# Kernel tuning notes

Hardware: AMD Instinct MI355X
Metric: run time of the kernel (lower is better)

## Reference

```python
import jax, jax.numpy as jnp
import numpy as np

B, V, FIN, K, FOUT, E = 8, 100000, 32, 4, 64, 800000


def setup_inputs() -> dict:
    key = jax.random.key(0)
    ks = jax.random.split(key, 6)
    inputs = jax.random.normal(ks[0], (B, V, FIN), dtype=jnp.float32)
    lap_rows = jax.random.randint(ks[1], (E,), 0, V, dtype=jnp.int32)
    lap_cols = jax.random.randint(ks[2], (E,), 0, V, dtype=jnp.int32)
    # rescaled-Laplacian nonzeros; small magnitude keeps the Chebyshev recurrence stable
    lap_vals = jax.random.normal(ks[3], (E,), dtype=jnp.float32) * 0.1
    # Kaiming-normal init: std = sqrt(2 / (Fin * K)) as in reset_parameters()
    std = float(np.sqrt(2.0 / (FIN * K)))
    weight = jax.random.normal(ks[4], (FIN, K, FOUT), dtype=jnp.float32) * std
    bias = jax.random.normal(ks[5], (FOUT,), dtype=jnp.float32) * 0.01
    return dict(inputs=inputs, lap_rows=lap_rows, lap_cols=lap_cols,
                lap_vals=lap_vals, weight=weight, bias=bias)


def reference(inputs, lap_rows, lap_cols, lap_vals, weight, bias):
    # inputs: [B, V, Fin]; weight: [Fin, K, Fout]; Laplacian in COO form.
    Bn, Vn, Fin = inputs.shape
    _, Kn, Fout = weight.shape

    def spmm(x):  # x: [V, Fin, B] -> L @ x via gather + segment-sum over edges
        msgs = lap_vals[:, None, None] * x[lap_cols]  # [E, Fin, B]
        return jax.ops.segment_sum(msgs, lap_rows, num_segments=Vn)

    x0 = jnp.transpose(inputs, (1, 2, 0))  # [V, Fin, B]
    xs = [x0]
    if Kn > 1:
        x1 = spmm(x0)
        xs.append(x1)
    for _ in range(2, Kn):
        x2 = 2.0 * spmm(x1) - x0  # Chebyshev recurrence T_k = 2 L T_{k-1} - T_{k-2}
        xs.append(x2)
        x0, x1 = x1, x2
    x = jnp.stack(xs, axis=0)  # [K, V, Fin, B]
    out = jnp.einsum('kvfb,fko->bvo', x, weight) + bias  # [B, V, Fout]
    return out
```

## Files before the change

kernel.cpp:

```cpp
#include <hip/hip_runtime.h>
#include <hip/hip_bf16.h>

#define B_    8
#define V_    100000
#define FIN_  32
#define K_    4
#define FOUT_ 64
#define E_    800000
#define NODE_F 256

typedef __attribute__((ext_vector_type(8))) short bf16x8;
typedef __attribute__((ext_vector_type(4))) float floatx4;

static __device__ inline float bf2f(unsigned short u) {
    unsigned int x = ((unsigned int)u) << 16;
    return __builtin_bit_cast(float, x);
}
static __device__ inline unsigned short f2bf(float f) {
    __hip_bfloat16 h = __float2bfloat16(f);
    return __builtin_bit_cast(unsigned short, h);
}

__global__ __launch_bounds__(256) void k_transpose(const float* __restrict__ in,
                                                   unsigned short* __restrict__ x0,
                                                   const int* __restrict__ rows,
                                                   int* __restrict__ counts,
                                                   const float* __restrict__ weight,
                                                   unsigned short* __restrict__ wpack) {
    int tid = blockIdx.x * 256 + threadIdx.x;
    int f4 = tid & 7;
    int m  = tid >> 3;
    int v  = m >> 3;
    int b  = m & 7;
    float4 val = ((const float4*)(in + ((size_t)b * V_ + v) * FIN_))[f4];
    ushort4 o;
    o.x = f2bf(val.x); o.y = f2bf(val.y); o.z = f2bf(val.z); o.w = f2bf(val.w);
    ((ushort4*)x0)[tid] = o;

    if (tid < E_) atomicAdd(&counts[rows[tid]], 1);

    if (tid < 1024) {
        int lane = tid & 63;
        int ot   = (tid >> 6) & 3;
        int kq   = tid >> 8;
        int quad = lane >> 4, l16 = lane & 15;
        bf16x8 w;
        #pragma unroll
        for (int j = 0; j < 8; ++j)
            w[j] = (short)f2bf(weight[(size_t)(quad * 8 + j) * (K_ * FOUT_) + kq * FOUT_ + ot * 16 + l16]);
        *((bf16x8*)(wpack + (size_t)tid * 8)) = w;
    }
}

__global__ __launch_bounds__(256) void k_zero_int(int* __restrict__ p, int n) {
    int t = blockIdx.x * 256 + threadIdx.x;
    if (t < n) p[t] = 0;
}

__global__ __launch_bounds__(1024) void k_scan1(const int* __restrict__ counts,
                                                int* __restrict__ row_ptr,
                                                int* __restrict__ cursor,
                                                int* __restrict__ bsums, int n) {
    __shared__ int s[1024];
    int t = threadIdx.x;
    int idx = blockIdx.x * 1024 + t;
    int v = (idx < n) ? counts[idx] : 0;
    s[t] = v;
    __syncthreads();
    for (int off = 1; off < 1024; off <<= 1) {
        int add = (t >= off) ? s[t - off] : 0;
        __syncthreads();
        s[t] += add;
        __syncthreads();
    }
    if (idx < n) {
        int r = s[t] - v;
        row_ptr[idx] = r;
        cursor[idx]  = r;
    }
    if (t == 1023) bsums[blockIdx.x] = s[1023];
}

__global__ __launch_bounds__(128) void k_scan2(const int* __restrict__ bsums,
                                               int* __restrict__ boffs, int nb) {
    __shared__ int s[128];
    int t = threadIdx.x;
    int v = (t < nb) ? bsums[t] : 0;
    s[t] = v;
    __syncthreads();
    for (int off = 1; off < 128; off <<= 1) {
        int add = (t >= off) ? s[t - off] : 0;
        __syncthreads();
        s[t] += add;
        __syncthreads();
    }
    boffs[t] = s[t] - v;
}

__global__ __launch_bounds__(256) void k_scatter(const int* __restrict__ rows,
                                                 const int* __restrict__ cols,
                                                 const float* __restrict__ vals,
                                                 int* __restrict__ cursor,
                                                 const int* __restrict__ boffs,
                                                 int2* __restrict__ e_pack) {
    int e = blockIdx.x * 256 + threadIdx.x;
    if (e < E_) {
        int r = rows[e];
        int pos = atomicAdd(&cursor[r], 1) + boffs[r >> 10];
        e_pack[pos] = make_int2(cols[e], __float_as_int(vals[e]));
    }
}

static __device__ inline void spmm_row(const unsigned short* __restrict__ xc,
                                       const int2* __restrict__ ep,
                                       int beg, int end, int lane, float a[4]) {
    int e = beg;
    for (; e + 3 < end; e += 4) {
        int2 p0 = ep[e], p1 = ep[e + 1], p2 = ep[e + 2], p3 = ep[e + 3];
        ushort4 g0 = *((const ushort4*)(xc + (size_t)p0.x * NODE_F + lane * 4));
        ushort4 g1 = *((const ushort4*)(xc + (size_t)p1.x * NODE_F + lane * 4));
        ushort4 g2 = *((const ushort4*)(xc + (size_t)p2.x * NODE_F + lane * 4));
        ushort4 g3 = *((const ushort4*)(xc + (size_t)p3.x * NODE_F + lane * 4));
        float w0 = __int_as_float(p0.y), w1 = __int_as_float(p1.y);
        float w2 = __int_as_float(p2.y), w3 = __int_as_float(p3.y);
        a[0] += w0 * bf2f(g0.x); a[1] += w0 * bf2f(g0.y); a[2] += w0 * bf2f(g0.z); a[3] += w0 * bf2f(g0.w);
        a[0] += w1 * bf2f(g1.x); a[1] += w1 * bf2f(g1.y); a[2] += w1 * bf2f(g1.z); a[3] += w1 * bf2f(g1.w);
        a[0] += w2 * bf2f(g2.x); a[1] += w2 * bf2f(g2.y); a[2] += w2 * bf2f(g2.z); a[3] += w2 * bf2f(g2.w);
        a[0] += w3 * bf2f(g3.x); a[1] += w3 * bf2f(g3.y); a[2] += w3 * bf2f(g3.z); a[3] += w3 * bf2f(g3.w);
    }
    for (; e < end; ++e) {
        int2 p = ep[e];
        ushort4 g = *((const ushort4*)(xc + (size_t)p.x * NODE_F + lane * 4));
        float w = __int_as_float(p.y);
        a[0] += w * bf2f(g.x); a[1] += w * bf2f(g.y); a[2] += w * bf2f(g.z); a[3] += w * bf2f(g.w);
    }
}

__global__ __launch_bounds__(256) void k_spmm(const unsigned short* __restrict__ xc,
                                              const unsigned short* __restrict__ xp,
                                              const int* __restrict__ row_ptr,
                                              const int* __restrict__ boffs,
                                              const int2* __restrict__ ep,
                                              unsigned short* __restrict__ xn,
                                              float scale, int has_prev) {
    int wave = threadIdx.x >> 6;
    int lane = threadIdx.x & 63;
    int v = blockIdx.x * 4 + wave;
    if (v >= V_) return;
    int beg = row_ptr[v] + boffs[v >> 10];
    int end = (v == V_ - 1) ? E_ : row_ptr[v + 1] + boffs[(v + 1) >> 10];

    float a[4] = {0.f, 0.f, 0.f, 0.f};
    spmm_row(xc, ep, beg, end, lane, a);

    float r[4];
    if (has_prev) {
        ushort4 p = *((const ushort4*)(xp + (size_t)v * NODE_F + lane * 4));
        r[0] = scale * a[0] - bf2f(p.x);
        r[1] = scale * a[1] - bf2f(p.y);
        r[2] = scale * a[2] - bf2f(p.z);
        r[3] = scale * a[3] - bf2f(p.w);
    } else {
        r[0] = a[0]; r[1] = a[1]; r[2] = a[2]; r[3] = a[3];
    }
    ushort4 o;
    o.x = f2bf(r[0]); o.y = f2bf(r[1]); o.z = f2bf(r[2]); o.w = f2bf(r[3]);
    *((ushort4*)(xn + (size_t)v * NODE_F + lane * 4)) = o;
}

__global__ __launch_bounds__(256) void k_spmm3c(const unsigned short* __restrict__ x0,
                                                const unsigned short* __restrict__ x1,
                                                const unsigned short* __restrict__ x2,
                                                const int* __restrict__ row_ptr,
                                                const int* __restrict__ boffs,
                                                const int2* __restrict__ ep,
                                                const unsigned short* __restrict__ wpack,
                                                const float* __restrict__ bias,
                                                float* __restrict__ out) {
    __shared__ __align__(16) unsigned short x3s[4][2][NODE_F];
    int wave = threadIdx.x >> 6;
    int lane = threadIdx.x & 63;
    int quad = lane >> 4;
    int l16  = lane & 15;
    int pair = blockIdx.x * 4 + wave;
    int v0 = pair * 2;

    #pragma unroll 1
    for (int s = 0; s < 2; ++s) {
        int v = v0 + s;
        int beg = row_ptr[v] + boffs[v >> 10];
        int end = (v == V_ - 1) ? E_ : row_ptr[v + 1] + boffs[(v + 1) >> 10];
        float a[4] = {0.f, 0.f, 0.f, 0.f};
        spmm_row(x2, ep, beg, end, lane, a);
        ushort4 p1 = *((const ushort4*)(x1 + (size_t)v * NODE_F + lane * 4));
        ushort4 o;
        o.x = f2bf(2.f * a[0] - bf2f(p1.x));
        o.y = f2bf(2.f * a[1] - bf2f(p1.y));
        o.z = f2bf(2.f * a[2] - bf2f(p1.z));
        o.w = f2bf(2.f * a[3] - bf2f(p1.w));
        *((ushort4*)&x3s[wave][s][lane * 4]) = o;
    }
    __syncthreads();

    const unsigned short* xs012[3] = {x0, x1, x2};
    bf16x8 wfrag[4][4];
    #pragma unroll
    for (int kq = 0; kq < 4; ++kq)
        #pragma unroll
        for (int ot = 0; ot < 4; ++ot)
            wfrag[kq][ot] = *((const bf16x8*)(wpack + (size_t)((kq * 4 + ot) * 64 + lane) * 8));

    floatx4 acc[4];
    #pragma unroll
    for (int ot = 0; ot < 4; ++ot)
        acc[ot] = *((const floatx4*)(bias + ot * 16 + quad * 4));

    int m0 = pair * 16;
    #pragma unroll
    for (int kq = 0; kq < 4; ++kq) {
        bf16x8 xf;
        if (kq < 3)
            xf = *((const bf16x8*)(xs012[kq] + (size_t)(m0 + l16) * FIN_ + quad * 8));
        else
            xf = *((const bf16x8*)&x3s[wave][l16 >> 3][(l16 & 7) * FIN_ + quad * 8]);
        #pragma unroll
        for (int ot = 0; ot < 4; ++ot)
            acc[ot] = __builtin_amdgcn_mfma_f32_16x16x32_bf16(wfrag[kq][ot], xf, acc[ot], 0, 0, 0);
    }

    int m = m0 + l16;
    int v = m >> 3;
    int b = m & 7;
    float* op = out + ((size_t)b * V_ + v) * FOUT_ + quad * 4;
    #pragma unroll
    for (int ot = 0; ot < 4; ++ot)
        *((floatx4*)(op + ot * 16)) = acc[ot];
}

extern "C" void kernel_launch(void* const* d_in, const int* in_sizes, int n_in,
                              void* d_out, int out_size, void* d_ws, size_t ws_size,
                              hipStream_t stream) {
    const float* inputs  = (const float*)d_in[0];
    const int*   laprows = (const int*)d_in[1];
    const int*   lapcols = (const int*)d_in[2];
    const float* lapvals = (const float*)d_in[3];
    const float* weight  = (const float*)d_in[4];
    const float* bias    = (const float*)d_in[5];
    float* out = (float*)d_out;

    const size_t XN = (size_t)V_ * NODE_F;
    unsigned short* x0 = (unsigned short*)d_ws;
    unsigned short* x1 = x0 + XN;
    unsigned short* x2 = x1 + XN;
    int* counts  = (int*)(x2 + XN);
    int* row_ptr = counts + V_;
    int* cursor  = row_ptr + V_;
    int* bsums   = cursor + V_;
    int* boffs   = bsums + 128;
    int2* e_pack = (int2*)(boffs + 128);
    unsigned short* wpack = (unsigned short*)(e_pack + E_);

    const int NB_SCAN = (V_ + 1023) / 1024;

    hipLaunchKernelGGL(k_zero_int, dim3((V_ + 255) / 256), dim3(256), 0, stream, counts, V_);
    hipLaunchKernelGGL(k_transpose, dim3((V_ * B_ * 8) / 256), dim3(256), 0, stream,
                       inputs, x0, laprows, counts, weight, wpack);
    hipLaunchKernelGGL(k_scan1, dim3(NB_SCAN), dim3(1024), 0, stream,
                       counts, row_ptr, cursor, bsums, V_);
    hipLaunchKernelGGL(k_scan2, dim3(1), dim3(128), 0, stream, bsums, boffs, NB_SCAN);
    hipLaunchKernelGGL(k_scatter, dim3((E_ + 255) / 256), dim3(256), 0, stream,
                       laprows, lapcols, lapvals, cursor, boffs, e_pack);

    hipLaunchKernelGGL(k_spmm, dim3(V_ / 4), dim3(256), 0, stream,
                       x0, (const unsigned short*)nullptr, row_ptr, boffs, e_pack, x1, 1.0f, 0);
    hipLaunchKernelGGL(k_spmm, dim3(V_ / 4), dim3(256), 0, stream,
                       x1, x0, row_ptr, boffs, e_pack, x2, 2.0f, 1);

    hipLaunchKernelGGL(k_spmm3c, dim3(12500), dim3(256), 0, stream,
                       x0, x1, x2, row_ptr, boffs, e_pack, wpack, bias, out);
}
```

Baseline: 608.8 us.

## Gather int8-quantized node features with per-node scales in SpMM

Each Chebyshev term is additionally stored as int8 with a per-node scale (offset by 128), and the SpMM gathers read these int8 rows instead of bf16, halving gathered bytes per edge. The zero-point is removed through a running sum of scaled edge weights. Bf16 copies are still written for the dense MFMA stage and the previous-term subtraction. Output stores become nontemporal. This adds a wave-wide max reduction and extra writes per node, and lowers gather precision to 8 bits, which risks accuracy tolerance.

Result: faster. 582.7 us (-4.3%).

```diff
diff --git a/kernel.cpp b/kernel.cpp
--- a/kernel.cpp
+++ b/kernel.cpp
@@ -21,13 +21,39 @@
     return __builtin_bit_cast(unsigned short, h);
 }
 
+static __device__ inline float wave_max64(float m) {
+    #pragma unroll
+    for (int off = 1; off < 64; off <<= 1)
+        m = fmaxf(m, __shfl_xor(m, off));
+    return m;
+}
+
+static __device__ inline void quant_store(const float r[4], int v, int lane,
+                                          unsigned char* __restrict__ xi,
+                                          float* __restrict__ sc) {
+    float m = fmaxf(fmaxf(fabsf(r[0]), fabsf(r[1])), fmaxf(fabsf(r[2]), fabsf(r[3])));
+    m = wave_max64(m);
+    float inv = (m > 0.f) ? 127.f / m : 0.f;
+    if (lane == 0) sc[v] = (m > 0.f) ? m * (1.f / 127.f) : 0.f;
+    unsigned int q = 0;
+    #pragma unroll
+    for (int j = 0; j < 4; ++j) {
+        int qi = (int)rintf(r[j] * inv) + 128;
+        q |= ((unsigned int)(qi & 0xff)) << (8 * j);
+    }
+    ((unsigned int*)(xi + (size_t)v * NODE_F))[lane] = q;
+}
+
 __global__ __launch_bounds__(256) void k_transpose(const float* __restrict__ in,
                                                    unsigned short* __restrict__ x0,
+                                                   unsigned char* __restrict__ x0i,
+                                                   float* __restrict__ s0,
                                                    const int* __restrict__ rows,
                                                    int* __restrict__ counts,
                                                    const float* __restrict__ weight,
                                                    unsigned short* __restrict__ wpack) {
     int tid = blockIdx.x * 256 + threadIdx.x;
+    int lane = threadIdx.x & 63;
     int f4 = tid & 7;
     int m  = tid >> 3;
     int v  = m >> 3;
@@ -37,13 +63,16 @@
     o.x = f2bf(val.x); o.y = f2bf(val.y); o.z = f2bf(val.z); o.w = f2bf(val.w);
     ((ushort4*)x0)[tid] = o;
 
+    float r[4] = {val.x, val.y, val.z, val.w};
+    quant_store(r, v, lane, x0i, s0);
+
     if (tid < E_) atomicAdd(&counts[rows[tid]], 1);
 
     if (tid < 1024) {
-        int lane = tid & 63;
+        int l = tid & 63;
         int ot   = (tid >> 6) & 3;
         int kq   = tid >> 8;
-        int quad = lane >> 4, l16 = lane & 15;
+        int quad = l >> 4, l16 = l & 15;
         bf16x8 w;
         #pragma unroll
         for (int j = 0; j < 8; ++j)
@@ -111,66 +140,85 @@
     }
 }
 
-static __device__ inline void spmm_row(const unsigned short* __restrict__ xc,
-                                       const int2* __restrict__ ep,
-                                       int beg, int end, int lane, float a[4]) {
+static __device__ inline void spmm_row_i8(const unsigned char* __restrict__ xi,
+                                          const float* __restrict__ sc,
+                                          const int2* __restrict__ ep,
+                                          int beg, int end, int lane,
+                                          float a[4], float* swp) {
+    float sw = 0.f;
     int e = beg;
     for (; e + 3 < end; e += 4) {
         int2 p0 = ep[e], p1 = ep[e + 1], p2 = ep[e + 2], p3 = ep[e + 3];
-        ushort4 g0 = *((const ushort4*)(xc + (size_t)p0.x * NODE_F + lane * 4));
-        ushort4 g1 = *((const ushort4*)(xc + (size_t)p1.x * NODE_F + lane * 4));
-        ushort4 g2 = *((const ushort4*)(xc + (size_t)p2.x * NODE_F + lane * 4));
-        ushort4 g3 = *((const ushort4*)(xc + (size_t)p3.x * NODE_F + lane * 4));
-        float w0 = __int_as_float(p0.y), w1 = __int_as_float(p1.y);
-        float w2 = __int_as_float(p2.y), w3 = __int_as_float(p3.y);
-        a[0] += w0 * bf2f(g0.x); a[1] += w0 * bf2f(g0.y); a[2] += w0 * bf2f(g0.z); a[3] += w0 * bf2f(g0.w);
-        a[0] += w1 * bf2f(g1.x); a[1] += w1 * bf2f(g1.y); a[2] += w1 * bf2f(g1.z); a[3] += w1 * bf2f(g1.w);
-        a[0] += w2 * bf2f(g2.x); a[1] += w2 * bf2f(g2.y); a[2] += w2 * bf2f(g2.z); a[3] += w2 * bf2f(g2.w);
-        a[0] += w3 * bf2f(g3.x); a[1] += w3 * bf2f(g3.y); a[2] += w3 * bf2f(g3.z); a[3] += w3 * bf2f(g3.w);
+        unsigned int g0 = ((const unsigned int*)(xi + (size_t)p0.x * NODE_F))[lane];
+        unsigned int g1 = ((const unsigned int*)(xi + (size_t)p1.x * NODE_F))[lane];
+        unsigned int g2 = ((const unsigned int*)(xi + (size_t)p2.x * NODE_F))[lane];
+        unsigned int g3 = ((const unsigned int*)(xi + (size_t)p3.x * NODE_F))[lane];
+        float w0 = __int_as_float(p0.y) * sc[p0.x];
+        float w1 = __int_as_float(p1.y) * sc[p1.x];
+        float w2 = __int_as_float(p2.y) * sc[p2.x];
+        float w3 = __int_as_float(p3.y) * sc[p3.x];
+        sw += w0 + w1 + w2 + w3;
+        a[0] += w0 * (float)(g0 & 0xff);         a[1] += w0 * (float)((g0 >> 8) & 0xff);
+        a[2] += w0 * (float)((g0 >> 16) & 0xff); a[3] += w0 * (float)(g0 >> 24);
+        a[0] += w1 * (float)(g1 & 0xff);         a[1] += w1 * (float)((g1 >> 8) & 0xff);
+        a[2] += w1 * (float)((g1 >> 16) & 0xff); a[3] += w1 * (float)(g1 >> 24);
+        a[0] += w2 * (float)(g2 & 0xff);         a[1] += w2 * (float)((g2 >> 8) & 0xff);
+        a[2] += w2 * (float)((g2 >> 16) & 0xff); a[3] += w2 * (float)(g2 >> 24);
+        a[0] += w3 * (float)(g3 & 0xff);         a[1] += w3 * (float)((g3 >> 8) & 0xff);
+        a[2] += w3 * (float)((g3 >> 16) & 0xff); a[3] += w3 * (float)(g3 >> 24);
     }
     for (; e < end; ++e) {
         int2 p = ep[e];
-        ushort4 g = *((const ushort4*)(xc + (size_t)p.x * NODE_F + lane * 4));
-        float w = __int_as_float(p.y);
-        a[0] += w * bf2f(g.x); a[1] += w * bf2f(g.y); a[2] += w * bf2f(g.z); a[3] += w * bf2f(g.w);
-    }
-}
-
-__global__ __launch_bounds__(256) void k_spmm(const unsigned short* __restrict__ xc,
+        unsigned int g = ((const unsigned int*)(xi + (size_t)p.x * NODE_F))[lane];
+        float w = __int_as_float(p.y) * sc[p.x];
+        sw += w;
+        a[0] += w * (float)(g & 0xff);         a[1] += w * (float)((g >> 8) & 0xff);
+        a[2] += w * (float)((g >> 16) & 0xff); a[3] += w * (float)(g >> 24);
+    }
+    *swp = sw;
+}
+
+__global__ __launch_bounds__(256) void k_spmm(const unsigned char* __restrict__ xci,
+                                              const float* __restrict__ sci,
                                               const unsigned short* __restrict__ xp,
                                               const int* __restrict__ row_ptr,
                                               const int* __restrict__ boffs,
                                               const int2* __restrict__ ep,
                                               unsigned short* __restrict__ xn,
+                                              unsigned char* __restrict__ xni,
+                                              float* __restrict__ scn,
                                               float scale, int has_prev) {
     int wave = threadIdx.x >> 6;
     int lane = threadIdx.x & 63;
     int v = blockIdx.x * 4 + wave;
-    if (v >= V_) return;
     int beg = row_ptr[v] + boffs[v >> 10];
     int end = (v == V_ - 1) ? E_ : row_ptr[v + 1] + boffs[(v + 1) >> 10];
 
     float a[4] = {0.f, 0.f, 0.f, 0.f};
-    spmm_row(xc, ep, beg, end, lane, a);
+    float sw;
+    spmm_row_i8(xci, sci, ep, beg, end, lane, a, &sw);
 
     float r[4];
+    #pragma unroll
+    for (int j = 0; j < 4; ++j) r[j] = a[j] - 128.f * sw;
     if (has_prev) {
         ushort4 p = *((const ushort4*)(xp + (size_t)v * NODE_F + lane * 4));
-        r[0] = scale * a[0] - bf2f(p.x);
-        r[1] = scale * a[1] - bf2f(p.y);
-        r[2] = scale * a[2] - bf2f(p.z);
-        r[3] = scale * a[3] - bf2f(p.w);
-    } else {
-        r[0] = a[0]; r[1] = a[1]; r[2] = a[2]; r[3] = a[3];
+        r[0] = scale * r[0] - bf2f(p.x);
+        r[1] = scale * r[1] - bf2f(p.y);
+        r[2] = scale * r[2] - bf2f(p.z);
+        r[3] = scale * r[3] - bf2f(p.w);
     }
     ushort4 o;
     o.x = f2bf(r[0]); o.y = f2bf(r[1]); o.z = f2bf(r[2]); o.w = f2bf(r[3]);
     *((ushort4*)(xn + (size_t)v * NODE_F + lane * 4)) = o;
+    quant_store(r, v, lane, xni, scn);
 }
 
 __global__ __launch_bounds__(256) void k_spmm3c(const unsigned short* __restrict__ x0,
                                                 const unsigned short* __restrict__ x1,
                                                 const unsigned short* __restrict__ x2,
+                                                const unsigned char* __restrict__ x2i,
+                                                const float* __restrict__ s2,
                                                 const int* __restrict__ row_ptr,
                                                 const int* __restrict__ boffs,
                                                 const int2* __restrict__ ep,
@@ -191,13 +239,14 @@
         int beg = row_ptr[v] + boffs[v >> 10];
         int end = (v == V_ - 1) ? E_ : row_ptr[v + 1] + boffs[(v + 1) >> 10];
         float a[4] = {0.f, 0.f, 0.f, 0.f};
-        spmm_row(x2, ep, beg, end, lane, a);
+        float sw;
+        spmm_row_i8(x2i, s2, ep, beg, end, lane, a, &sw);
         ushort4 p1 = *((const ushort4*)(x1 + (size_t)v * NODE_F + lane * 4));
         ushort4 o;
-        o.x = f2bf(2.f * a[0] - bf2f(p1.x));
-        o.y = f2bf(2.f * a[1] - bf2f(p1.y));
-        o.z = f2bf(2.f * a[2] - bf2f(p1.z));
-        o.w = f2bf(2.f * a[3] - bf2f(p1.w));
+        o.x = f2bf(2.f * (a[0] - 128.f * sw) - bf2f(p1.x));
+        o.y = f2bf(2.f * (a[1] - 128.f * sw) - bf2f(p1.y));
+        o.z = f2bf(2.f * (a[2] - 128.f * sw) - bf2f(p1.z));
+        o.w = f2bf(2.f * (a[3] - 128.f * sw) - bf2f(p1.w));
         *((ushort4*)&x3s[wave][s][lane * 4]) = o;
     }
     __syncthreads();
@@ -234,7 +283,7 @@
     float* op = out + ((size_t)b * V_ + v) * FOUT_ + quad * 4;
     #pragma unroll
     for (int ot = 0; ot < 4; ++ot)
-        *((floatx4*)(op + ot * 16)) = acc[ot];
+        __builtin_nontemporal_store(acc[ot], (floatx4*)(op + ot * 16));
 }
 
 extern "C" void kernel_launch(void* const* d_in, const int* in_sizes, int n_in,
@@ -248,23 +297,30 @@
     const float* bias    = (const float*)d_in[5];
     float* out = (float*)d_out;
 
-    const size_t XN = (size_t)V_ * NODE_F;
+    const size_t XN  = (size_t)V_ * NODE_F;
+    const size_t XNI = (size_t)V_ * NODE_F;
     unsigned short* x0 = (unsigned short*)d_ws;
     unsigned short* x1 = x0 + XN;
     unsigned short* x2 = x1 + XN;
-    int* counts  = (int*)(x2 + XN);
+    unsigned char* x0i = (unsigned char*)(x2 + XN);
+    unsigned char* x1i = x0i + XNI;
+    unsigned char* x2i = x1i + XNI;
+    float* s0 = (float*)(x2i + XNI);
+    float* s1 = s0 + V_;
+    float* s2 = s1 + V_;
+    int* counts  = (int*)(s2 + V_);
     int* row_ptr = counts + V_;
     int* cursor  = row_ptr + V_;
     int* bsums   = cursor + V_;
     int* boffs   = bsums + 128;
-    int2* e_pack = (int2*)(boffs + 128);
-    unsigned short* wpack = (unsigned short*)(e_pack + E_);
+    unsigned short* wpack = (unsigned short*)(boffs + 128);
+    int2* e_pack = (int2*)(wpack + 8192);
 
     const int NB_SCAN = (V_ + 1023) / 1024;
 
     hipLaunchKernelGGL(k_zero_int, dim3((V_ + 255) / 256), dim3(256), 0, stream, counts, V_);
     hipLaunchKernelGGL(k_transpose, dim3((V_ * B_ * 8) / 256), dim3(256), 0, stream,
-                       inputs, x0, laprows, counts, weight, wpack);
+                       inputs, x0, x0i, s0, laprows, counts, weight, wpack);
     hipLaunchKernelGGL(k_scan1, dim3(NB_SCAN), dim3(1024), 0, stream,
                        counts, row_ptr, cursor, bsums, V_);
     hipLaunchKernelGGL(k_scan2, dim3(1), dim3(128), 0, stream, bsums, boffs, NB_SCAN);
@@ -272,10 +328,12 @@
                        laprows, lapcols, lapvals, cursor, boffs, e_pack);
 
     hipLaunchKernelGGL(k_spmm, dim3(V_ / 4), dim3(256), 0, stream,
-                       x0, (const unsigned short*)nullptr, row_ptr, boffs, e_pack, x1, 1.0f, 0);
+                       x0i, s0, (const unsigned short*)nullptr, row_ptr, boffs, e_pack,
+                       x1, x1i, s1, 1.0f, 0);
     hipLaunchKernelGGL(k_spmm, dim3(V_ / 4), dim3(256), 0, stream,
-                       x1, x0, row_ptr, boffs, e_pack, x2, 2.0f, 1);
+                       x1i, s1, x0, row_ptr, boffs, e_pack,
+                       x2, x2i, s2, 2.0f, 1);
 
     hipLaunchKernelGGL(k_spmm3c, dim3(12500), dim3(256), 0, stream,
-                       x0, x1, x2, row_ptr, boffs, e_pack, wpack, bias, out);
-}
+                       x0, x1, x2, x2i, s2, row_ptr, boffs, e_pack, wpack, bias, out);
+}
```
